# Optimization experiments

Measured on AMD Instinct MI355X. Metric: run time of the kernel, lower is better.

Reference implementation:

```python
import jax, jax.numpy as jnp
import numpy as np

N = 8192
IN_DIM = 256
HID = 256
OUT_DIM = 256
P_DIM = 3
SIGMA = 1.0


def setup_inputs() -> dict:
    key = jax.random.key(0)
    ks = jax.random.split(key, 7)
    s_in = 1.0 / np.sqrt(IN_DIM)
    inp = {
        "X": jax.random.normal(ks[0], (N, IN_DIM + P_DIM), dtype=jnp.float32),
        "WQ": jax.random.uniform(ks[1], (IN_DIM, HID), jnp.float32, -s_in, s_in),
        "bQ": jax.random.uniform(ks[2], (HID,), jnp.float32, -s_in, s_in),
        "WK": jax.random.uniform(ks[3], (IN_DIM, HID), jnp.float32, -s_in, s_in),
        "bK": jax.random.uniform(ks[4], (HID,), jnp.float32, -s_in, s_in),
        "WV": jax.random.uniform(ks[5], (IN_DIM, OUT_DIM), jnp.float32, -s_in, s_in),
        "bV": jax.random.uniform(ks[6], (OUT_DIM,), jnp.float32, -s_in, s_in),
    }
    return inp


def _softmax_one(x):
    # exp(x - max) / (1 + sum(exp(x - max))) -- faithful to the torch softmax_one
    m = jnp.max(x, axis=-1, keepdims=True)
    e = jnp.exp(x - m)
    return e / (1.0 + jnp.sum(e, axis=-1, keepdims=True))


def reference(X, WQ, bQ, WK, bK, WV, bV):
    P = X[:, -P_DIM:]            # [N, 3] spatial coords
    Xf = X[:, :-P_DIM]           # [N, IN_DIM] features

    Q = Xf @ WQ + bQ             # [N, HID]
    K = Xf @ WK + bK             # [N, HID]
    V = Xf @ WV + bV             # [N, OUT_DIM]

    scores = (Q @ K.T) / jnp.sqrt(jnp.asarray(HID, Xf.dtype))  # [N, N]

    # squared pairwise distances ||P_i - P_j||^2 (cdist(P,P)**2)
    sq = jnp.sum(P * P, axis=-1)                                # [N]
    d2 = jnp.maximum(sq[:, None] + sq[None, :] - 2.0 * (P @ P.T), 0.0)
    decay = jnp.exp(-d2 / (2.0 * SIGMA ** 2))                   # [N, N]

    A = _softmax_one(scores * decay)                             # [N, N]
    H = A @ V                                                    # [N, OUT_DIM]
    # residual: input_dim == output_dim so res_proj is None
    return H + Xf
```

## Files before the change

### kernel.cpp

```cpp
#include <hip/hip_runtime.h>
#include <hip/hip_bf16.h>
#include <stdint.h>

#define NTOK 8192
#define XSTRIDE 259
#define LOG2E 1.4426950408889634f
#define DECC (-3.4712336270551023f)
#define KSPLIT 8
#define SPLEN (NTOK / KSPLIT)
#define BN 64
#define ITERS (SPLEN / BN)

typedef __bf16 bf16x8 __attribute__((ext_vector_type(8)));
typedef float f32x4 __attribute__((ext_vector_type(4)));
typedef float f32x16 __attribute__((ext_vector_type(16)));
typedef unsigned short u16;

union BF8 { u16 u[8]; bf16x8 v; };
union PW  { uint32_t u[4]; bf16x8 v; };

__device__ __forceinline__ u16 f2bf(float f) {
  uint32_t u = __float_as_uint(f);
  u += 0x7FFFu + ((u >> 16) & 1u);
  return (u16)(u >> 16);
}
__device__ __forceinline__ float bf2f(u16 h) {
  return __uint_as_float(((uint32_t)h) << 16);
}
__device__ __forceinline__ float exp2_hw(float x) {
  float r; asm("v_exp_f32 %0, %1" : "=v"(r) : "v"(x)); return r;
}
__device__ __forceinline__ f32x4 mfma16(bf16x8 a, bf16x8 b, f32x4 c) {
  return __builtin_amdgcn_mfma_f32_16x16x32_bf16(a, b, c, 0, 0, 0);
}
__device__ __forceinline__ f32x16 mfma32(bf16x8 a, bf16x8 b, f32x16 c) {
  return __builtin_amdgcn_mfma_f32_32x32x16_bf16(a, b, c, 0, 0, 0);
}
__device__ __forceinline__ void async16(const void* g, void* l) {
  __builtin_amdgcn_global_load_lds(
      (const __attribute__((address_space(1))) uint32_t*)g,
      (__attribute__((address_space(3))) uint32_t*)l, 16, 0, 0);
}
__device__ __forceinline__ void bsplit(float v, u16& h, u16& l) {
  h = f2bf(v);
  l = f2bf(v - bf2f(h));
}

__global__ __launch_bounds__(256) void prep_kernel(
    const float* __restrict__ X, const float* __restrict__ WQ,
    const float* __restrict__ WK, const float* __restrict__ WV,
    u16* __restrict__ Xb, u16* __restrict__ Qp, u16* __restrict__ Kp,
    u16* __restrict__ Wt) {
  const int bid = blockIdx.x;
  const int t = threadIdx.x;
  if (bid < NTOK / 8) {
    const int row = bid * 8 + (t >> 5);
    const int c0 = (t & 31) * 8;
    const float* xp = X + (size_t)row * XSTRIDE + c0;
    union { u16 u[8]; uint4 v; } o;
#pragma unroll
    for (int j = 0; j < 8; ++j) o.u[j] = f2bf(xp[j]);
    *(uint4*)(Xb + (size_t)row * 256 + c0) = o.v;

    if (t < 8) {
      const int r = bid * 8 + t;
      const float* pp = X + (size_t)r * XSTRIDE + 256;
      const float x = pp[0], y = pp[1], z = pp[2];
      const float w = 0.5f * (x * x + y * y + z * z);
      u16 xh, xl, yh, yl, zh, zl, wh, wl;
      bsplit(x, xh, xl); bsplit(y, yh, yl); bsplit(z, zh, zl);
      bsplit(w, wh, wl);
      const u16 one = 0x3F80u;
      const u16 SGN = 0x8000u;
      union { u16 u[16]; uint4 v4[2]; } uq, uk;
      uq.u[0] = wh;  uk.u[0] = one;
      uq.u[1] = wl;  uk.u[1] = one;
      uq.u[2] = one; uk.u[2] = wh;
      uq.u[3] = one; uk.u[3] = wl;
      uq.u[4] = (u16)(xh ^ SGN); uk.u[4] = xh;
      uq.u[5] = (u16)(xh ^ SGN); uk.u[5] = xl;
      uq.u[6] = (u16)(xl ^ SGN); uk.u[6] = xh;
      uq.u[7] = (u16)(yh ^ SGN); uk.u[7] = yh;
      uq.u[8] = (u16)(yh ^ SGN); uk.u[8] = yl;
      uq.u[9] = (u16)(yl ^ SGN); uk.u[9] = yh;
      uq.u[10] = (u16)(zh ^ SGN); uk.u[10] = zh;
      uq.u[11] = (u16)(zh ^ SGN); uk.u[11] = zl;
      uq.u[12] = (u16)(zl ^ SGN); uk.u[12] = zh;
      uq.u[13] = 0; uk.u[13] = 0;
      uq.u[14] = 0; uk.u[14] = 0;
      uq.u[15] = 0; uk.u[15] = 0;
      ((uint4*)Qp)[r * 2] = uq.v4[0];
      ((uint4*)Qp)[r * 2 + 1] = uq.v4[1];
      ((uint4*)Kp)[r * 2] = uk.v4[0];
      ((uint4*)Kp)[r * 2 + 1] = uk.v4[1];
    }
  } else {
    __shared__ u16 T[32 * 264];
    const int b2 = bid - NTOK / 8;
    const int which = b2 >> 3, ob = b2 & 7;
    const float* W = (which == 0) ? WQ : ((which == 1) ? WK : WV);
    const int kk = t >> 5, oo = t & 31;
#pragma unroll
    for (int kc = 0; kc < 32; ++kc) {
      const int k = kc * 8 + kk;
      T[oo * 264 + k] = f2bf(W[(size_t)k * 256 + ob * 32 + oo]);
    }
    __syncthreads();
#pragma unroll
    for (int i = 0; i < 4; ++i) {
      int chn = i * 256 + t;
      int o2 = chn >> 5, s = chn & 31;
      uint4 d = *(const uint4*)(T + o2 * 264 + s * 8);
      *(uint4*)(Wt + (size_t)(which * 256 + ob * 32 + o2) * 256 + s * 8) = d;
    }
  }
}

__global__ __launch_bounds__(256) void qkv_kernel(
    const u16* __restrict__ Xb, const u16* __restrict__ Wt,
    const float* __restrict__ bQ, const float* __restrict__ bK,
    const float* __restrict__ bV,
    u16* __restrict__ Qb, u16* __restrict__ Kb, u16* __restrict__ Vt) {
  __shared__ u16 wt[2][64 * 256];
  const int tid = threadIdx.x;
  const int lane = tid & 63;
  const int wave = tid >> 6;
  const int l15 = lane & 15;
  const int q4 = lane >> 4;
  const int rb = blockIdx.x;
  const int which = blockIdx.y;
  const float* bias = (which == 0) ? bQ : ((which == 1) ? bK : bV);
  const int grow0 = rb * 64;

  bf16x8 xa[8];
  {
    const int row = grow0 + wave * 16 + l15;
#pragma unroll
    for (int kc = 0; kc < 8; ++kc)
      xa[kc] = *(const bf16x8*)(Xb + (size_t)row * 256 + kc * 32 + q4 * 8);
  }

#define STAGEW(C_, B_)                                                        \
  do {                                                                        \
    const u16* Wsrc = Wt + (size_t)(which * 256 + (C_) * 64) * 256;           \
    const int rb0 = wave * 16;                                                \
    _Pragma("unroll")                                                         \
    for (int i = 0; i < 8; ++i) {                                             \
      int r = rb0 + i * 2 + (lane >> 5);                                      \
      int cc = (lane & 31) ^ (r & 7);                                         \
      async16(Wsrc + (size_t)r * 256 + cc * 8, &wt[B_][(rb0 + i * 2) * 256]); \
    }                                                                         \
  } while (0)

  STAGEW(0, 0);

#pragma unroll 1
  for (int c = 0; c < 4; ++c) {
    const int cur = c & 1;
    const int c0 = c * 64;
    asm volatile("s_waitcnt vmcnt(0)" ::: "memory");
    __syncthreads();
    if (c < 3) STAGEW(c + 1, cur ^ 1);

    f32x4 acc[4];
#pragma unroll
    for (int nt = 0; nt < 4; ++nt) acc[nt] = (f32x4){0.f, 0.f, 0.f, 0.f};
#pragma unroll
    for (int kc = 0; kc < 8; ++kc) {
#pragma unroll
      for (int nt = 0; nt < 4; ++nt) {
        bf16x8 wf = *(const bf16x8*)(&wt[cur][(nt * 16 + l15) * 256 +
                                     (((kc * 4 + q4) ^ (l15 & 7)) * 8)]);
        acc[nt] = mfma16(xa[kc], wf, acc[nt]);
      }
    }
    float bc[4];
#pragma unroll
    for (int nt = 0; nt < 4; ++nt) bc[nt] = bias[c0 + nt * 16 + l15];

    __syncthreads();
    u16* smem = &wt[cur][0];

    if (which == 2) {
#pragma unroll
      for (int nt = 0; nt < 4; ++nt) {
        const int lcol = nt * 16 + l15;
        union { u16 u[4]; uint2 w; } p;
#pragma unroll
        for (int r = 0; r < 4; ++r) p.u[r] = f2bf(acc[nt][r] + bc[nt]);
        *(uint2*)(smem + lcol * 72 + wave * 16 + q4 * 4) = p.w;
      }
      __syncthreads();
#pragma unroll
      for (int i = 0; i < 2; ++i) {
        int chn = i * 256 + tid;
        int lcol = chn >> 3, s = chn & 7;
        uint4 d = *(const uint4*)(smem + lcol * 72 + s * 8);
        *(uint4*)(Vt + (size_t)(c0 + lcol) * NTOK + grow0 + s * 8) = d;
      }
    } else {
#pragma unroll
      for (int nt = 0; nt < 4; ++nt)
#pragma unroll
        for (int r = 0; r < 4; ++r)
          smem[(wave * 16 + q4 * 4 + r) * 72 + nt * 16 + l15] =
              f2bf(acc[nt][r] + bc[nt]);
      __syncthreads();
#pragma unroll
      for (int i = 0; i < 2; ++i) {
        int chn = i * 256 + tid;
        int lrow = chn >> 3, g = chn & 7;
        uint4 d = *(const uint4*)(smem + lrow * 72 + g * 8);
        int grow = grow0 + lrow, gc = c0 + g * 8;
        if (which == 1)
          *(uint4*)(Kb + (size_t)grow * 256 + gc) = d;
        else
          *(uint4*)(Qb + (size_t)((grow >> 5) * 16 + (gc >> 4)) * 512 +
                    ((gc >> 3) & 1) * 256 + (grow & 31) * 8) = d;
      }
    }
  }
#undef STAGEW
}

__global__ __launch_bounds__(512, 2) void attn_kernel(
    const u16* __restrict__ Qb, const u16* __restrict__ Kb,
    const u16* __restrict__ Vt, const u16* __restrict__ Qp,
    const u16* __restrict__ Kp, u16* __restrict__ Op,
    float* __restrict__ ml) {
  __shared__ u16 kbuf[2][BN * 256];
  __shared__ u16 vbuf[2][256 * BN];
  __shared__ u16 kpbuf[2][BN * 16];

  const int tid = threadIdx.x;
  const int lane = tid & 63;
  const int wave = tid >> 6;
  const int l31 = lane & 31;
  const int h5 = lane >> 5;
  const int sp = blockIdx.x;
  const int rb = blockIdx.y;
  const int q0 = rb * 256;
  const int wrow = wave * 32;

#define STAGE(T, S_)                                                          \
  do {                                                                        \
    const int key0_ = sp * SPLEN + (T) * BN;                                  \
    _Pragma("unroll")                                                         \
    for (int j = 0; j < 4; ++j) {                                             \
      int r = wave * 8 + j * 2 + (lane >> 5);                                 \
      int c = (lane & 31) ^ (r & 7);                                          \
      async16(Kb + (size_t)(key0_ + r) * 256 + c * 8,                         \
              &kbuf[S_][(wave * 8 + j * 2) * 256]);                           \
    }                                                                         \
    _Pragma("unroll")                                                         \
    for (int j = 0; j < 4; ++j) {                                             \
      int f = wave * 32 + j * 8 + (lane >> 3);                                \
      int c = (lane & 7) ^ (f & 7);                                           \
      async16(Vt + (size_t)f * NTOK + key0_ + c * 8,                          \
              &vbuf[S_][(wave * 32 + j * 8) * BN]);                           \
    }                                                                         \
    if (wave == 0) {                                                          \
      _Pragma("unroll")                                                       \
      for (int hh = 0; hh < 2; ++hh)                                          \
        async16(Kp + (size_t)(key0_ + hh * 32 + (lane >> 1)) * 16 +           \
                    (lane & 1) * 8,                                           \
                &kpbuf[S_][hh * 32 * 16]);                                    \
    }                                                                         \
  } while (0)

  const int rb32 = rb * 8 + wave;
  bf16x8 qa[16];
#pragma unroll
  for (int kc = 0; kc < 16; ++kc)
    qa[kc] = *(const bf16x8*)(Qb + ((size_t)(rb32 * 16 + kc) * 64 + lane) * 8);

  const bf16x8 qp = *(const bf16x8*)(Qp + (size_t)(q0 + wrow + l31) * 16 +
                                     h5 * 8);

  f32x16 O[8];
#pragma unroll
  for (int ft = 0; ft < 8; ++ft)
#pragma unroll
    for (int r = 0; r < 16; ++r) O[ft][r] = 0.f;
  float lrow = 0.f;

  const int swz = l31 & 7;

  STAGE(0, 0);

#pragma unroll 1
  for (int t = 0; t < ITERS; ++t) {
    const int slot = t & 1;
    asm volatile("s_waitcnt vmcnt(0)" ::: "memory");
    __builtin_amdgcn_s_barrier();
    if (t + 1 < ITERS) STAGE(t + 1, slot ^ 1);

#pragma unroll
    for (int sub = 0; sub < 2; ++sub) {
      f32x16 T;
#pragma unroll
      for (int r = 0; r < 16; ++r) T[r] = 0.f;
      {
        bf16x8 kpf = *(const bf16x8*)(&kpbuf[slot][(sub * 32 + l31) * 16 +
                                      h5 * 8]);
        T = mfma32(kpf, qp, T);
      }

      f32x16 S;
#pragma unroll
      for (int r = 0; r < 16; ++r) S[r] = 0.f;
      __builtin_amdgcn_s_setprio(1);
#pragma unroll
      for (int kc = 0; kc < 16; ++kc) {
        bf16x8 kf = *(const bf16x8*)(&kbuf[slot][(sub * 32 + l31) * 256 +
                                     (((2 * kc + h5) ^ swz) * 8)]);
        S = mfma32(kf, qa[kc], S);
      }
      __builtin_amdgcn_s_setprio(0);

#pragma unroll
      for (int r = 0; r < 16; ++r) {
        float dec = exp2_hw(fmaf(T[r], -LOG2E, DECC));
        float p = exp2_hw(S[r] * dec);
        S[r] = p;
        lrow += p;
      }

      uint32_t w0, w1, w2, w3, w4, w5, w6, w7;
      asm("v_cvt_pk_bf16_f32 %0, %1, %2" : "=v"(w0) : "v"(S[0]),  "v"(S[1]));
      asm("v_cvt_pk_bf16_f32 %0, %1, %2" : "=v"(w1) : "v"(S[2]),  "v"(S[3]));
      asm("v_cvt_pk_bf16_f32 %0, %1, %2" : "=v"(w2) : "v"(S[4]),  "v"(S[5]));
      asm("v_cvt_pk_bf16_f32 %0, %1, %2" : "=v"(w3) : "v"(S[6]),  "v"(S[7]));
      asm("v_cvt_pk_bf16_f32 %0, %1, %2" : "=v"(w4) : "v"(S[8]),  "v"(S[9]));
      asm("v_cvt_pk_bf16_f32 %0, %1, %2" : "=v"(w5) : "v"(S[10]), "v"(S[11]));
      asm("v_cvt_pk_bf16_f32 %0, %1, %2" : "=v"(w6) : "v"(S[12]), "v"(S[13]));
      asm("v_cvt_pk_bf16_f32 %0, %1, %2" : "=v"(w7) : "v"(S[14]), "v"(S[15]));
      asm volatile("v_permlane32_swap_b32 %0, %1" : "+v"(w2), "+v"(w0));
      asm volatile("v_permlane32_swap_b32 %0, %1" : "+v"(w3), "+v"(w1));
      asm volatile("v_permlane32_swap_b32 %0, %1" : "+v"(w6), "+v"(w4));
      asm volatile("v_permlane32_swap_b32 %0, %1" : "+v"(w7), "+v"(w5));
      PW pa0, pa1;
      pa0.u[0] = w0; pa0.u[1] = w1; pa0.u[2] = w2; pa0.u[3] = w3;
      pa1.u[0] = w4; pa1.u[1] = w5; pa1.u[2] = w6; pa1.u[3] = w7;

      __builtin_amdgcn_s_setprio(1);
#pragma unroll
      for (int kh = 0; kh < 2; ++kh) {
        const bf16x8 pa = kh ? pa1.v : pa0.v;
        const int khh = sub * 2 + kh;
#pragma unroll
        for (int ft = 0; ft < 8; ++ft) {
          bf16x8 vf = *(const bf16x8*)(&vbuf[slot][(ft * 32 + l31) * BN +
                                       (((2 * khh + h5) ^ swz) * 8)]);
          O[ft] = mfma32(pa, vf, O[ft]);
        }
      }
      __builtin_amdgcn_s_setprio(0);
    }
  }

  float lsum = lrow + __shfl_xor(lrow, 32);
#pragma unroll
  for (int ft = 0; ft < 8; ++ft)
#pragma unroll
    for (int r = 0; r < 16; ++r) {
      int row = q0 + wrow + (r & 3) + 8 * (r >> 2) + 4 * h5;
      Op[((size_t)sp * NTOK + row) * 256 + ft * 32 + l31] = f2bf(O[ft][r]);
    }
  if (lane < 32)
    ml[sp * NTOK + q0 + wrow + lane] = lsum;
#undef STAGE
}

__global__ __launch_bounds__(256) void combine_kernel(
    const float* __restrict__ X, const u16* __restrict__ Op,
    const float* __restrict__ ml, float* __restrict__ out) {
  const int row = blockIdx.x * 2 + (threadIdx.x >> 7);
  const int f2 = threadIdx.x & 127;
  float den = 1.f, n0 = 0.f, n1 = 0.f;
#pragma unroll
  for (int s = 0; s < KSPLIT; ++s) {
    den += ml[s * NTOK + row];
    uint32_t v = *(const uint32_t*)(Op + ((size_t)s * NTOK + row) * 256 +
                                    f2 * 2);
    n0 += bf2f((u16)v);
    n1 += bf2f((u16)(v >> 16));
  }
  const float inv = 1.f / den;
  float2 o;
  o.x = n0 * inv + X[(size_t)row * XSTRIDE + f2 * 2];
  o.y = n1 * inv + X[(size_t)row * XSTRIDE + f2 * 2 + 1];
  *(float2*)(out + (size_t)row * 256 + f2 * 2) = o;
}

extern "C" void kernel_launch(void* const* d_in, const int* in_sizes, int n_in,
                              void* d_out, int out_size, void* d_ws, size_t ws_size,
                              hipStream_t stream) {
  (void)in_sizes; (void)n_in; (void)out_size; (void)ws_size;
  const float* X  = (const float*)d_in[0];
  const float* WQ = (const float*)d_in[1];
  const float* bQ = (const float*)d_in[2];
  const float* WK = (const float*)d_in[3];
  const float* bK = (const float*)d_in[4];
  const float* WV = (const float*)d_in[5];
  const float* bV = (const float*)d_in[6];
  float* out = (float*)d_out;
  char* ws = (char*)d_ws;

  u16*   Qb = (u16*)(ws);
  u16*   Kb = (u16*)(ws + ((size_t)4 << 20));
  u16*   Vt = (u16*)(ws + ((size_t)8 << 20));
  u16*   Qp = (u16*)(ws + ((size_t)12 << 20));
  u16*   Kp = (u16*)(ws + ((size_t)12 << 20) + 262144);
  u16*   Wt = (u16*)(ws + ((size_t)12 << 20) + 524288);
  u16*   Xb = (u16*)(ws + ((size_t)12 << 20) + 524288 + 393216);
  float* ml = (float*)(ws + ((size_t)16 << 20) + 524288 + 393216);
  u16*   Op = (u16*)(ws + ((size_t)16 << 20) + 524288 + 393216 + 524288);

  prep_kernel<<<dim3(NTOK / 8 + 24), dim3(256), 0, stream>>>(
      X, WQ, WK, WV, Xb, Qp, Kp, Wt);
  qkv_kernel<<<dim3(128, 3), dim3(256), 0, stream>>>(Xb, Wt, bQ, bK, bV,
                                                     Qb, Kb, Vt);
  attn_kernel<<<dim3(KSPLIT, NTOK / 256), dim3(512), 0, stream>>>(
      Qb, Kb, Vt, Qp, Kp, Op, ml);
  combine_kernel<<<dim3(NTOK / 2), dim3(256), 0, stream>>>(X, Op, ml, out);
}
```

Measured before the change: 200.7 us.

## Fuse split-K combine into attention tail and convert X inside QKV kernel

Removes the separate combine kernel. The last split block for each row block, found with an atomic counter, reduces the partial outputs and writes the final result plus residual. The prep kernel no longer writes a bf16 copy of X; the QKV kernel reads fp32 X directly and converts it in registers. Prep shrinks to 56 blocks, which also reset the counters. This saves one launch and the Xb round trip, but the reduction is now serialised onto a few tail blocks and X reads are strided fp32.

```diff
diff --git a/kernel.cpp b/kernel.cpp
--- a/kernel.cpp
+++ b/kernel.cpp
@@ -49,55 +49,13 @@
 __global__ __launch_bounds__(256) void prep_kernel(
     const float* __restrict__ X, const float* __restrict__ WQ,
     const float* __restrict__ WK, const float* __restrict__ WV,
-    u16* __restrict__ Xb, u16* __restrict__ Qp, u16* __restrict__ Kp,
-    u16* __restrict__ Wt) {
+    u16* __restrict__ Qp, u16* __restrict__ Kp, u16* __restrict__ Wt,
+    int* __restrict__ cnt) {
   const int bid = blockIdx.x;
   const int t = threadIdx.x;
-  if (bid < NTOK / 8) {
-    const int row = bid * 8 + (t >> 5);
-    const int c0 = (t & 31) * 8;
-    const float* xp = X + (size_t)row * XSTRIDE + c0;
-    union { u16 u[8]; uint4 v; } o;
-#pragma unroll
-    for (int j = 0; j < 8; ++j) o.u[j] = f2bf(xp[j]);
-    *(uint4*)(Xb + (size_t)row * 256 + c0) = o.v;
-
-    if (t < 8) {
-      const int r = bid * 8 + t;
-      const float* pp = X + (size_t)r * XSTRIDE + 256;
-      const float x = pp[0], y = pp[1], z = pp[2];
-      const float w = 0.5f * (x * x + y * y + z * z);
-      u16 xh, xl, yh, yl, zh, zl, wh, wl;
-      bsplit(x, xh, xl); bsplit(y, yh, yl); bsplit(z, zh, zl);
-      bsplit(w, wh, wl);
-      const u16 one = 0x3F80u;
-      const u16 SGN = 0x8000u;
-      union { u16 u[16]; uint4 v4[2]; } uq, uk;
-      uq.u[0] = wh;  uk.u[0] = one;
-      uq.u[1] = wl;  uk.u[1] = one;
-      uq.u[2] = one; uk.u[2] = wh;
-      uq.u[3] = one; uk.u[3] = wl;
-      uq.u[4] = (u16)(xh ^ SGN); uk.u[4] = xh;
-      uq.u[5] = (u16)(xh ^ SGN); uk.u[5] = xl;
-      uq.u[6] = (u16)(xl ^ SGN); uk.u[6] = xh;
-      uq.u[7] = (u16)(yh ^ SGN); uk.u[7] = yh;
-      uq.u[8] = (u16)(yh ^ SGN); uk.u[8] = yl;
-      uq.u[9] = (u16)(yl ^ SGN); uk.u[9] = yh;
-      uq.u[10] = (u16)(zh ^ SGN); uk.u[10] = zh;
-      uq.u[11] = (u16)(zh ^ SGN); uk.u[11] = zl;
-      uq.u[12] = (u16)(zl ^ SGN); uk.u[12] = zh;
-      uq.u[13] = 0; uk.u[13] = 0;
-      uq.u[14] = 0; uk.u[14] = 0;
-      uq.u[15] = 0; uk.u[15] = 0;
-      ((uint4*)Qp)[r * 2] = uq.v4[0];
-      ((uint4*)Qp)[r * 2 + 1] = uq.v4[1];
-      ((uint4*)Kp)[r * 2] = uk.v4[0];
-      ((uint4*)Kp)[r * 2 + 1] = uk.v4[1];
-    }
-  } else {
+  if (bid < 24) {
     __shared__ u16 T[32 * 264];
-    const int b2 = bid - NTOK / 8;
-    const int which = b2 >> 3, ob = b2 & 7;
+    const int which = bid >> 3, ob = bid & 7;
     const float* W = (which == 0) ? WQ : ((which == 1) ? WK : WV);
     const int kk = t >> 5, oo = t & 31;
 #pragma unroll
@@ -113,11 +71,42 @@
       uint4 d = *(const uint4*)(T + o2 * 264 + s * 8);
       *(uint4*)(Wt + (size_t)(which * 256 + ob * 32 + o2) * 256 + s * 8) = d;
     }
+  } else {
+    if (bid == 24 && t < 32) cnt[t] = 0;
+    const int r = (bid - 24) * 256 + t;
+    const float* pp = X + (size_t)r * XSTRIDE + 256;
+    const float x = pp[0], y = pp[1], z = pp[2];
+    const float w = 0.5f * (x * x + y * y + z * z);
+    u16 xh, xl, yh, yl, zh, zl, wh, wl;
+    bsplit(x, xh, xl); bsplit(y, yh, yl); bsplit(z, zh, zl); bsplit(w, wh, wl);
+    const u16 one = 0x3F80u;
+    const u16 SGN = 0x8000u;
+    union { u16 u[16]; uint4 v4[2]; } uq, uk;
+    uq.u[0] = wh;  uk.u[0] = one;
+    uq.u[1] = wl;  uk.u[1] = one;
+    uq.u[2] = one; uk.u[2] = wh;
+    uq.u[3] = one; uk.u[3] = wl;
+    uq.u[4] = (u16)(xh ^ SGN); uk.u[4] = xh;
+    uq.u[5] = (u16)(xh ^ SGN); uk.u[5] = xl;
+    uq.u[6] = (u16)(xl ^ SGN); uk.u[6] = xh;
+    uq.u[7] = (u16)(yh ^ SGN); uk.u[7] = yh;
+    uq.u[8] = (u16)(yh ^ SGN); uk.u[8] = yl;
+    uq.u[9] = (u16)(yl ^ SGN); uk.u[9] = yh;
+    uq.u[10] = (u16)(zh ^ SGN); uk.u[10] = zh;
+    uq.u[11] = (u16)(zh ^ SGN); uk.u[11] = zl;
+    uq.u[12] = (u16)(zl ^ SGN); uk.u[12] = zh;
+    uq.u[13] = 0; uk.u[13] = 0;
+    uq.u[14] = 0; uk.u[14] = 0;
+    uq.u[15] = 0; uk.u[15] = 0;
+    ((uint4*)Qp)[r * 2] = uq.v4[0];
+    ((uint4*)Qp)[r * 2 + 1] = uq.v4[1];
+    ((uint4*)Kp)[r * 2] = uk.v4[0];
+    ((uint4*)Kp)[r * 2 + 1] = uk.v4[1];
   }
 }
 
 __global__ __launch_bounds__(256) void qkv_kernel(
-    const u16* __restrict__ Xb, const u16* __restrict__ Wt,
+    const float* __restrict__ X, const u16* __restrict__ Wt,
     const float* __restrict__ bQ, const float* __restrict__ bK,
     const float* __restrict__ bV,
     u16* __restrict__ Qb, u16* __restrict__ Kb, u16* __restrict__ Vt) {
@@ -135,9 +124,14 @@
   bf16x8 xa[8];
   {
     const int row = grow0 + wave * 16 + l15;
-#pragma unroll
-    for (int kc = 0; kc < 8; ++kc)
-      xa[kc] = *(const bf16x8*)(Xb + (size_t)row * 256 + kc * 32 + q4 * 8);
+    const float* xp = X + (size_t)row * XSTRIDE;
+#pragma unroll
+    for (int kc = 0; kc < 8; ++kc) {
+      BF8 u;
+#pragma unroll
+      for (int j = 0; j < 8; ++j) u.u[j] = f2bf(xp[kc * 32 + q4 * 8 + j]);
+      xa[kc] = u.v;
+    }
   }
 
 #define STAGEW(C_, B_)                                                        \
@@ -227,10 +221,13 @@
     const u16* __restrict__ Qb, const u16* __restrict__ Kb,
     const u16* __restrict__ Vt, const u16* __restrict__ Qp,
     const u16* __restrict__ Kp, u16* __restrict__ Op,
-    float* __restrict__ ml) {
+    float* __restrict__ ml, const float* __restrict__ X,
+    float* __restrict__ out, int* __restrict__ cnt) {
   __shared__ u16 kbuf[2][BN * 256];
   __shared__ u16 vbuf[2][256 * BN];
   __shared__ u16 kpbuf[2][BN * 16];
+  __shared__ float sden[256];
+  __shared__ int sh_flag;
 
   const int tid = threadIdx.x;
   const int lane = tid & 63;
@@ -369,28 +366,41 @@
     }
   if (lane < 32)
     ml[sp * NTOK + q0 + wrow + lane] = lsum;
+
+  __threadfence();
+  if (tid == 0) sh_flag = atomicAdd(&cnt[rb], 1);
+  __syncthreads();
+  if (sh_flag == KSPLIT - 1) {
+    __threadfence();
+    for (int r0 = tid; r0 < 256; r0 += 512) {
+      float den = 1.f;
+#pragma unroll
+      for (int s = 0; s < KSPLIT; ++s) den += ml[s * NTOK + q0 + r0];
+      sden[r0] = 1.f / den;
+    }
+    __syncthreads();
+#pragma unroll 1
+    for (int i = 0; i < 64; ++i) {
+      int idx = i * 512 + tid;
+      int lr = idx >> 7;
+      int f2 = idx & 127;
+      int row = q0 + lr;
+      float n0 = 0.f, n1 = 0.f;
+#pragma unroll
+      for (int s = 0; s < KSPLIT; ++s) {
+        uint32_t v = *(const uint32_t*)(Op + ((size_t)s * NTOK + row) * 256 +
+                                        f2 * 2);
+        n0 += bf2f((u16)v);
+        n1 += bf2f((u16)(v >> 16));
+      }
+      const float inv = sden[lr];
+      float2 o;
+      o.x = n0 * inv + X[(size_t)row * XSTRIDE + f2 * 2];
+      o.y = n1 * inv + X[(size_t)row * XSTRIDE + f2 * 2 + 1];
+      *(float2*)(out + (size_t)row * 256 + f2 * 2) = o;
+    }
+  }
 #undef STAGE
-}
-
-__global__ __launch_bounds__(256) void combine_kernel(
-    const float* __restrict__ X, const u16* __restrict__ Op,
-    const float* __restrict__ ml, float* __restrict__ out) {
-  const int row = blockIdx.x * 2 + (threadIdx.x >> 7);
-  const int f2 = threadIdx.x & 127;
-  float den = 1.f, n0 = 0.f, n1 = 0.f;
-#pragma unroll
-  for (int s = 0; s < KSPLIT; ++s) {
-    den += ml[s * NTOK + row];
-    uint32_t v = *(const uint32_t*)(Op + ((size_t)s * NTOK + row) * 256 +
-                                    f2 * 2);
-    n0 += bf2f((u16)v);
-    n1 += bf2f((u16)(v >> 16));
-  }
-  const float inv = 1.f / den;
-  float2 o;
-  o.x = n0 * inv + X[(size_t)row * XSTRIDE + f2 * 2];
-  o.y = n1 * inv + X[(size_t)row * XSTRIDE + f2 * 2 + 1];
-  *(float2*)(out + (size_t)row * 256 + f2 * 2) = o;
 }
 
 extern "C" void kernel_launch(void* const* d_in, const int* in_sizes, int n_in,
@@ -413,15 +423,14 @@
   u16*   Qp = (u16*)(ws + ((size_t)12 << 20));
   u16*   Kp = (u16*)(ws + ((size_t)12 << 20) + 262144);
   u16*   Wt = (u16*)(ws + ((size_t)12 << 20) + 524288);
-  u16*   Xb = (u16*)(ws + ((size_t)12 << 20) + 524288 + 393216);
   float* ml = (float*)(ws + ((size_t)16 << 20) + 524288 + 393216);
+  int*   cnt = (int*)(ws + ((size_t)16 << 20) + 524288 + 393216 + 262144);
   u16*   Op = (u16*)(ws + ((size_t)16 << 20) + 524288 + 393216 + 524288);
 
-  prep_kernel<<<dim3(NTOK / 8 + 24), dim3(256), 0, stream>>>(
-      X, WQ, WK, WV, Xb, Qp, Kp, Wt);
-  qkv_kernel<<<dim3(128, 3), dim3(256), 0, stream>>>(Xb, Wt, bQ, bK, bV,
+  prep_kernel<<<dim3(56), dim3(256), 0, stream>>>(X, WQ, WK, WV,
+                                                  Qp, Kp, Wt, cnt);
+  qkv_kernel<<<dim3(128, 3), dim3(256), 0, stream>>>(X, Wt, bQ, bK, bV,
                                                      Qb, Kb, Vt);
   attn_kernel<<<dim3(KSPLIT, NTOK / 256), dim3(512), 0, stream>>>(
-      Qb, Kb, Vt, Qp, Kp, Op, ml);
-  combine_kernel<<<dim3(NTOK / 2), dim3(256), 0, stream>>>(X, Op, ml, out);
-}
+      Qb, Kb, Vt, Qp, Kp, Op, ml, X, out, cnt);
+}
```

New measurement: 284.8 us. 41.9% more time.
